# Kernel tuning notes

Measured on AMD Instinct MI355X. Metric: run time of the kernel, lower is better.

The kernel has to match this reference:

```python
import jax, jax.numpy as jnp
import numpy as np

N = 4096          # total atoms
N_METAL = 1024    # first N_METAL atoms are metal (Z=79) by construction
L = 24.0          # cubic cell edge (Angstrom)
DL = 2.4
NK = 10           # int(L / DL) -- static k-grid extent per axis
SIGMA = 1.0 / 1.805132
SCALING = 1.0
FOUR_PI = 4.0 * np.pi

# static integer reciprocal grid with k=0 removed: (K,3), K = (2*NK+1)^3 - 1
_g = np.arange(-NK, NK + 1)
_INTS = np.stack(np.meshgrid(_g, _g, _g, indexing="ij"), axis=-1).reshape(-1, 3)
_INTS = _INTS[np.any(_INTS != 0, axis=1)].astype(np.float32)


def _ewald_potential(r, q, cell):
    """Reciprocal-space Ewald potential at each atom position.
    r: (n,3) positions, q: (n,m) charges (m charge columns), cell: (3,3)
    rows = lattice vectors. Returns (n,m) potential ('field' f in cace).
    pot_i = (4*pi/V) * sum_k exp(-sigma^2 k^2/2)/k^2 * Re[S(k) e^{-ik.r_i}]."""
    recip = (2.0 * np.pi) * jnp.linalg.inv(cell).T      # rows b1,b2,b3
    k = jnp.asarray(_INTS, dtype=r.dtype) @ recip       # (K,3)
    k2 = jnp.sum(k * k, axis=1)                         # (K,)
    kfac = jnp.exp((-0.5 * SIGMA * SIGMA) * k2) / k2    # (K,)
    vol = jnp.abs(jnp.linalg.det(cell))
    kr = r @ k.T                                        # (n,K)  dominant alloc
    c, s = jnp.cos(kr), jnp.sin(kr)
    sf_c = c.T @ q                                      # (K,m) structure factors
    sf_s = s.T @ q
    pot = c @ (kfac[:, None] * sf_c) + s @ (kfac[:, None] * sf_s)
    return (FOUR_PI / vol) * pot


def setup_inputs() -> dict:
    key = jax.random.key(0)
    k1, k2 = jax.random.split(key)
    positions = jax.random.uniform(k1, (N, 3), dtype=jnp.float32) * L
    q = jax.random.normal(k2, (N, 1), dtype=jnp.float32) * 0.1
    cell = (L * jnp.eye(3, dtype=jnp.float32)).reshape(1, 3, 3)
    atomic_numbers = jnp.concatenate([
        jnp.full((N_METAL,), 79, dtype=jnp.int32),   # metal block first
        jnp.full((N - N_METAL,), 8, dtype=jnp.int32),
    ])
    batch = jnp.zeros((N,), dtype=jnp.int32)         # single system
    return {"positions": positions, "q": q, "cell": cell,
            "atomic_numbers": atomic_numbers, "batch": batch}


def reference(positions, q, cell, atomic_numbers, batch):
    # single batch (batch all zeros); metal atoms are the first N_METAL
    # (atomic_numbers == 79 by construction, so the boolean mask is static)
    cell0 = cell.reshape(3, 3)
    q = q.at[:N_METAL].set(0.0)                      # q_all[metal] = 0
    r_m = positions[:N_METAL]

    # _compute_S_matrix: pairwise Ewald kernel among metal atoms via q=eye
    A = _ewald_potential(r_m, jnp.eye(N_METAL, dtype=positions.dtype), cell0)
    coeffs = jnp.ones((N_METAL + 1, N_METAL + 1), dtype=positions.dtype)
    coeffs = coeffs.at[:N_METAL, :N_METAL].set(A)
    coeffs = coeffs.at[N_METAL, N_METAL].set(0.0)
    S = jnp.linalg.inv(coeffs)                       # cached AJl in torch code

    # field at every atom from all (electrolyte) charges
    f = _ewald_potential(positions, q, cell0)        # (N,1)

    # external_field is None -> B_ext = 0, no external energy
    B = -f[:N_METAL] * SCALING                       # (N_METAL,1)
    chi = jnp.concatenate([B, jnp.zeros((1, 1), dtype=B.dtype)], axis=0)
    sol = S @ chi                                    # (N_METAL+1,1)
    q_mw = q.at[:N_METAL].set(sol[:-1] / SCALING)
    return q_mw
```

## Files before the change

### kernel.cpp

```cpp
#include <hip/hip_runtime.h>
#include <math.h>

#define NATOM 4096
#define NM    1024
#define NKR   9260
#define KSPLIT 14
#define CHPS  22
#define NCH   308
#define KC    32
#define KPAD2 9856
#define PI_F  3.14159265358979f

typedef short v8s __attribute__((ext_vector_type(8)));
typedef float v4f __attribute__((ext_vector_type(4)));

static __device__ __forceinline__ void kdata(int t, const float* __restrict__ cell,
                                             float& kxx, float& kyy, float& kzz, float& w) {
  if (t >= NKR) { kxx = 0.f; kyy = 0.f; kzz = 0.f; w = 0.f; return; }
  int u = (t < 4630) ? t : t + 1;
  int a = u / 441;
  int rem = u - a * 441;
  int b = rem / 21;
  int c = rem - b * 21;
  float na = (float)(a - 10), nb = (float)(b - 10), nc = (float)(c - 10);
  float m00=cell[0], m01=cell[1], m02=cell[2];
  float m10=cell[3], m11=cell[4], m12=cell[5];
  float m20=cell[6], m21=cell[7], m22=cell[8];
  float det = m00*(m11*m22 - m12*m21) - m01*(m10*m22 - m12*m20) + m02*(m10*m21 - m11*m20);
  float inv00 =  (m11*m22 - m12*m21) / det;
  float inv01 = -(m01*m22 - m02*m21) / det;
  float inv02 =  (m01*m12 - m02*m11) / det;
  float inv10 = -(m10*m22 - m12*m20) / det;
  float inv11 =  (m00*m22 - m02*m20) / det;
  float inv12 = -(m00*m12 - m02*m10) / det;
  float inv20 =  (m10*m21 - m11*m20) / det;
  float inv21 = -(m00*m21 - m01*m20) / det;
  float inv22 =  (m00*m11 - m01*m10) / det;
  const float twopi = 2.f * PI_F;
  kxx = twopi * (na*inv00 + nb*inv01 + nc*inv02);
  kyy = twopi * (na*inv10 + nb*inv11 + nc*inv12);
  kzz = twopi * (na*inv20 + nb*inv21 + nc*inv22);
  float k2 = kxx*kxx + kyy*kyy + kzz*kzz;
  const float sigma = 1.0f / 1.805132f;
  w = (4.f * PI_F / fabsf(det)) * __expf(-0.5f * sigma * sigma * k2) / k2;
}

__global__ __launch_bounds__(256)
void sfk(const float* __restrict__ pos, const float* __restrict__ q,
         const float* __restrict__ cell,
         float* __restrict__ kx, float* __restrict__ ky,
         float* __restrict__ kz, float* __restrict__ ksw,
         float* __restrict__ gc, float* __restrict__ gs) {
  __shared__ float red1[8][32], red2[8][32];
  const int kloc = threadIdx.x & 31;
  const int part = threadIdx.x >> 5;
  const int k = blockIdx.x * 32 + kloc;
  float kxx, kyy, kzz, w;
  kdata(k, cell, kxx, kyy, kzz, w);
  if (part == 0) { kx[k]=kxx; ky[k]=kyy; kz[k]=kzz; ksw[k]=sqrtf(w); }
  float sc = 0.f, ss = 0.f;
  const int j0 = NM + part * 384, j1 = j0 + 384;
  for (int j = j0; j < j1; ++j) {
    float kr = kxx*pos[3*j] + kyy*pos[3*j+1] + kzz*pos[3*j+2];
    float s, c;
    __sincosf(kr, &s, &c);
    float qj = q[j];
    sc += qj * c;
    ss += qj * s;
  }
  red1[part][kloc] = sc;
  red2[part][kloc] = ss;
  __syncthreads();
  if (part == 0) {
    float tc = 0.f, ts = 0.f;
    #pragma unroll
    for (int pp = 0; pp < 8; ++pp) { tc += red1[pp][kloc]; ts += red2[pp][kloc]; }
    gc[k] = w * tc;
    gs[k] = w * ts;
  }
}

__global__ __launch_bounds__(256)
void fB(const float* __restrict__ pos,
        const float* __restrict__ kx, const float* __restrict__ ky,
        const float* __restrict__ kz,
        const float* __restrict__ gc, const float* __restrict__ gs,
        float* __restrict__ r1, float* __restrict__ r2) {
  int i = blockIdx.x;
  float px = pos[3*i], py = pos[3*i+1], pz = pos[3*i+2];
  float p = 0.f;
  for (int k = threadIdx.x; k < KPAD2; k += 256) {
    float kr = kx[k]*px + ky[k]*py + kz[k]*pz;
    float s, c;
    __sincosf(kr, &s, &c);
    p += gc[k]*c + gs[k]*s;
  }
  for (int o = 32; o > 0; o >>= 1) p += __shfl_down(p, o, 64);
  __shared__ float red[4];
  if ((threadIdx.x & 63) == 0) red[threadIdx.x >> 6] = p;
  __syncthreads();
  if (threadIdx.x == 0) {
    r1[i] = -(red[0] + red[1] + red[2] + red[3]);
    r2[i] = 1.f;
  }
}

#define PSTR 40
__global__ __launch_bounds__(256, 2)
void gemmA(const float* __restrict__ pos,
           const float* __restrict__ kx, const float* __restrict__ ky,
           const float* __restrict__ kz, const float* __restrict__ ksw,
           float* __restrict__ A) {
  __shared__ short Pl[8][128 * PSTR];
  const int blk = blockIdx.x;
  const int split = blk / 36;
  const int tt = blk - split * 36;
  int bi = 0, rem = tt;
  while (rem >= 8 - bi) { rem -= 8 - bi; ++bi; }
  const int bj = bi + rem;
  const int t = threadIdx.x;
  const int side = t >> 7;
  const int a = t & 127;
  const int atom = (side ? bj : bi) * 128 + a;
  const float px = pos[3*atom], py = pos[3*atom+1], pz = pos[3*atom+2];
  const int axor = (a >> 3) & 3;
  short* PC_hi = &Pl[side*4+0][a*PSTR];
  short* PC_mi = &Pl[side*4+1][a*PSTR];
  short* PS_hi = &Pl[side*4+2][a*PSTR];
  short* PS_mi = &Pl[side*4+3][a*PSTR];

  const int w = t >> 6;
  const int lane = t & 63;
  const int ln15 = lane & 15;
  const int quad = lane >> 4;

  v4f acc[2][8];
  #pragma unroll
  for (int mt = 0; mt < 2; ++mt)
    #pragma unroll
    for (int nt = 0; nt < 8; ++nt) {
      v4f z = {0.f, 0.f, 0.f, 0.f};
      acc[mt][nt] = z;
    }

  for (int ch = split * CHPS; ch < split * CHPS + CHPS; ++ch) {
    const int kb = ch * KC;
    #pragma unroll
    for (int g = 0; g < 4; ++g) {
      v8s vch, vcm, vsh, vsm;
      #pragma unroll
      for (int j = 0; j < 8; ++j) {
        const int gk = kb + g*8 + j;
        float kr = kx[gk]*px + ky[gk]*py + kz[gk]*pz;
        float s, c;
        __sincosf(kr, &s, &c);
        float sw = ksw[gk];
        float cv = c * sw, sv = s * sw;
        unsigned cu = __float_as_uint(cv);
        float chf = __uint_as_float(cu & 0xffff0000u);
        unsigned cmu = __float_as_uint(cv - chf);
        unsigned su = __float_as_uint(sv);
        float shf = __uint_as_float(su & 0xffff0000u);
        unsigned smu = __float_as_uint(sv - shf);
        vch[j] = (short)(cu >> 16);
        vcm[j] = (short)(cmu >> 16);
        vsh[j] = (short)(su >> 16);
        vsm[j] = (short)(smu >> 16);
      }
      const int slot = (g ^ axor) * 8;
      *(v8s*)&PC_hi[slot] = vch;
      *(v8s*)&PC_mi[slot] = vcm;
      *(v8s*)&PS_hi[slot] = vsh;
      *(v8s*)&PS_mi[slot] = vsm;
    }
    __syncthreads();
    v8s aCh[2], aCm[2], aSh[2], aSm[2];
    #pragma unroll
    for (int mt = 0; mt < 2; ++mt) {
      const int row = w*32 + mt*16 + ln15;
      const int off = row * PSTR + (quad ^ ((row >> 3) & 3)) * 8;
      aCh[mt] = *(const v8s*)&Pl[0][off];
      aCm[mt] = *(const v8s*)&Pl[1][off];
      aSh[mt] = *(const v8s*)&Pl[2][off];
      aSm[mt] = *(const v8s*)&Pl[3][off];
    }
    #pragma unroll
    for (int nt = 0; nt < 8; ++nt) {
      const int row = nt*16 + ln15;
      const int off = row * PSTR + (quad ^ ((row >> 3) & 3)) * 8;
      v8s bCh = *(const v8s*)&Pl[4][off];
      v8s bCm = *(const v8s*)&Pl[5][off];
      v8s bSh = *(const v8s*)&Pl[6][off];
      v8s bSm = *(const v8s*)&Pl[7][off];
      #pragma unroll
      for (int mt = 0; mt < 2; ++mt) {
        v4f d = acc[mt][nt];
        d = __builtin_amdgcn_mfma_f32_16x16x32_bf16(aCh[mt], bCh, d, 0, 0, 0);
        d = __builtin_amdgcn_mfma_f32_16x16x32_bf16(aCh[mt], bCm, d, 0, 0, 0);
        d = __builtin_amdgcn_mfma_f32_16x16x32_bf16(aCm[mt], bCh, d, 0, 0, 0);
        d = __builtin_amdgcn_mfma_f32_16x16x32_bf16(aSh[mt], bSh, d, 0, 0, 0);
        d = __builtin_amdgcn_mfma_f32_16x16x32_bf16(aSh[mt], bSm, d, 0, 0, 0);
        d = __builtin_amdgcn_mfma_f32_16x16x32_bf16(aSm[mt], bSh, d, 0, 0, 0);
        acc[mt][nt] = d;
      }
    }
    __syncthreads();
  }
  #pragma unroll
  for (int mt = 0; mt < 2; ++mt)
    #pragma unroll
    for (int nt = 0; nt < 8; ++nt)
      #pragma unroll
      for (int r = 0; r < 4; ++r) {
        const int row = bi*128 + w*32 + mt*16 + quad*4 + r;
        const int col = bj*128 + nt*16 + ln15;
        atomicAdd(&A[row*1024 + col], acc[mt][nt][r]);
      }
}

__global__ __launch_bounds__(256)
void step(float* __restrict__ A, const float* __restrict__ r1, const float* __restrict__ r2,
          float* __restrict__ ru1, float* __restrict__ ru2,
          float* __restrict__ y1g, float* __restrict__ y2g, int p) {
  __shared__ __align__(16) float D[32][36];
  __shared__ __align__(16) float T[32][36];
  __shared__ float yp1[32], yp2[32];
  const int t = threadIdx.x;
  const int nb = 32 - p;
  const int i0 = (t >> 4) * 2, j0 = (t & 15) * 2;
  const int lr = t >> 3, lc = (t & 7) * 4;

  if ((int)blockIdx.x >= nb) {
    int rem = blockIdx.x - nb, a = 0;
    while (rem >= a + 1) { rem -= (a + 1); ++a; }
    const int qi = p + 1 + a, qj = p + 1 + rem;
    *(v4f*)&D[lr][lc] = *(const v4f*)&A[(qi*32+lr)*1024 + (p-1)*32 + lc];
    *(v4f*)&T[lr][lc] = *(const v4f*)&A[(qj*32+lr)*1024 + (p-1)*32 + lc];
    float o[2][2];
    if (p == 1 && (qi >> 2) != (qj >> 2)) {
      #pragma unroll
      for (int ii = 0; ii < 2; ++ii)
        #pragma unroll
        for (int jj = 0; jj < 2; ++jj)
          o[ii][jj] = A[(qj*32 + j0+jj)*1024 + qi*32 + i0+ii];
    } else {
      #pragma unroll
      for (int ii = 0; ii < 2; ++ii)
        #pragma unroll
        for (int jj = 0; jj < 2; ++jj)
          o[ii][jj] = A[(qi*32+i0+ii)*1024 + qj*32 + j0+jj];
    }
    __syncthreads();
    for (int m = 0; m < 32; ++m) {
      float a0 = D[i0][m], a1 = D[i0+1][m];
      float b0 = T[j0][m], b1 = T[j0+1][m];
      o[0][0]-=a0*b0; o[0][1]-=a0*b1;
      o[1][0]-=a1*b0; o[1][1]-=a1*b1;
    }
    #pragma unroll
    for (int ii = 0; ii < 2; ++ii)
      #pragma unroll
      for (int jj = 0; jj < 2; ++jj)
        A[(qi*32+i0+ii)*1024 + qj*32 + j0+jj] = o[ii][jj];
    return;
  }

  const int b = blockIdx.x;
  const int q = p + b;
  float rv1 = 0.f, rv2 = 0.f;
  if (p >= 1 && t < 32) { yp1[t] = y1g[(p-1)*32 + t]; yp2[t] = y2g[(p-1)*32 + t]; }
  if (p == 0) {
    *(v4f*)&D[lr][lc] = *(const v4f*)&A[lr*1024 + lc];
    if (b > 0) {
      if (q < 4) {
        *(v4f*)&T[lr][lc] = *(const v4f*)&A[(q*32+lr)*1024 + lc];
      } else {
        for (int e = t; e < 1024; e += 256)
          T[e&31][e>>5] = A[(e>>5)*1024 + q*32 + (e&31)];
      }
    }
    __syncthreads();
    if (b == 0 && t < 32) { rv1 = r1[t]; rv2 = r2[t]; }
  } else {
    *(v4f*)&D[lr][lc] = *(const v4f*)&A[(p*32+lr)*1024 + (p-1)*32 + lc];
    if (b > 0)
      *(v4f*)&T[lr][lc] = *(const v4f*)&A[(q*32+lr)*1024 + (p-1)*32 + lc];
    __syncthreads();
    if (t < 32) {
      if (b == 0) {
        float a1 = 0.f, a2 = 0.f;
        for (int j = 0; j < 32; ++j) {
          float lv = D[t][j];
          a1 += lv * yp1[j];
          a2 += lv * yp2[j];
        }
        rv1 = r1[p*32 + t] - a1;
        rv2 = r2[p*32 + t] - a2;
      } else {
        float a1 = 0.f, a2 = 0.f;
        for (int j = 0; j < 32; ++j) {
          float lv = T[t][j];
          a1 += lv * yp1[j];
          a2 += lv * yp2[j];
        }
        ru1[q*32 + t] -= a1;
        ru2[q*32 + t] -= a2;
      }
    }
    float o1[2][2];
    #pragma unroll
    for (int ii = 0; ii < 2; ++ii)
      #pragma unroll
      for (int jj = 0; jj < 2; ++jj)
        o1[ii][jj] = A[(p*32+i0+ii)*1024 + p*32 + j0+jj];
    for (int m = 0; m < 32; ++m) {
      float a0 = D[i0][m], a1 = D[i0+1][m];
      float b0 = D[j0][m], b1 = D[j0+1][m];
      o1[0][0]-=a0*b0; o1[0][1]-=a0*b1;
      o1[1][0]-=a1*b0; o1[1][1]-=a1*b1;
    }
    float o2[2][2];
    if (b > 0) {
      if (p == 1 && (q >> 2) != 0) {
        #pragma unroll
        for (int ii = 0; ii < 2; ++ii)
          #pragma unroll
          for (int jj = 0; jj < 2; ++jj)
            o2[ii][jj] = A[(1*32 + j0+jj)*1024 + q*32 + i0+ii];
      } else {
        #pragma unroll
        for (int ii = 0; ii < 2; ++ii)
          #pragma unroll
          for (int jj = 0; jj < 2; ++jj)
            o2[ii][jj] = A[(q*32+i0+ii)*1024 + p*32 + j0+jj];
      }
      for (int m = 0; m < 32; ++m) {
        float a0 = T[i0][m], a1 = T[i0+1][m];
        float b0 = D[j0][m], b1 = D[j0+1][m];
        o2[0][0]-=a0*b0; o2[0][1]-=a0*b1;
        o2[1][0]-=a1*b0; o2[1][1]-=a1*b1;
      }
    }
    __syncthreads();
    #pragma unroll
    for (int ii = 0; ii < 2; ++ii)
      #pragma unroll
      for (int jj = 0; jj < 2; ++jj)
        D[i0+ii][j0+jj] = o1[ii][jj];
    if (b > 0) {
      #pragma unroll
      for (int ii = 0; ii < 2; ++ii)
        #pragma unroll
        for (int jj = 0; jj < 2; ++jj)
          T[i0+ii][j0+jj] = o2[ii][jj];
    }
    __syncthreads();
  }

  if (t < 32) {
    float a[32];
    #pragma unroll
    for (int m = 0; m < 32; ++m) a[m] = D[t][m];
    #pragma unroll
    for (int j = 0; j < 32; ++j) {
      float dj = __shfl(a[j], j);
      float rinv = rsqrtf(dj);
      float lj = (t == j) ? dj * rinv : a[j] * rinv;
      a[j] = lj;
      #pragma unroll
      for (int m = j + 1; m < 32; ++m)
        a[m] -= lj * __shfl(lj, m);
    }
    #pragma unroll
    for (int m = 0; m < 32; ++m) D[t][m] = a[m];
  }
  __syncthreads();
  if (b == 0) {
    for (int e = t; e < 1024; e += 256) {
      int i = e >> 5, j = e & 31;
      if (i >= j) A[(p*32+i)*1024 + p*32 + j] = D[i][j];
    }
    if (t < 32) {
      float v1 = rv1, v2 = rv2;
      for (int j = 0; j < 32; ++j) {
        float invd = 1.f / D[j][j];
        float Lij = D[t][j];
        float x1 = __shfl(v1, j) * invd;
        float x2 = __shfl(v2, j) * invd;
        if (t == j)      { v1 = x1; v2 = x2; }
        else if (t > j)  { v1 -= Lij * x1; v2 -= Lij * x2; }
      }
      y1g[p*32 + t] = v1; y2g[p*32 + t] = v2;
    }
  } else {
    if (t < 32) {
      #pragma unroll
      for (int cb = 0; cb < 2; ++cb) {
        const int cbase = cb * 16;
        float x[16];
        #pragma unroll
        for (int k = 0; k < 16; ++k) x[k] = T[t][cbase + k];
        for (int m = 0; m < cbase; ++m) {
          float tm = T[t][m];
          #pragma unroll
          for (int k = 0; k < 16; ++k)
            x[k] -= tm * D[cbase + k][m];
        }
        #pragma unroll
        for (int k = 0; k < 16; ++k) {
          float xv = x[k] * (1.0f / D[cbase + k][cbase + k]);
          x[k] = xv;
          #pragma unroll
          for (int m2 = k + 1; m2 < 16; ++m2)
            x[m2] -= xv * D[cbase + m2][cbase + k];
        }
        #pragma unroll
        for (int k = 0; k < 16; ++k) T[t][cbase + k] = x[k];
      }
    }
    __syncthreads();
    *(v4f*)&A[(q*32+lr)*1024 + p*32 + lc] = *(const v4f*)&T[lr][lc];
  }
}

__global__ __launch_bounds__(64)
void invd(const float* __restrict__ A, float* __restrict__ iD) {
  __shared__ float Lb[64][65];
  __shared__ float Xs[64][65];
  const int k = blockIdx.x;
  const int j = threadIdx.x;
  const int base = k * 64;
  for (int e = j; e < 4096; e += 64) {
    int r = e >> 6, c = e & 63;
    Lb[r][c] = (r >= c) ? A[(base + r)*1024 + base + c] : 0.f;
  }
  __syncthreads();
  for (int r = 0; r < j; ++r) Xs[r][j] = 0.f;
  Xs[j][j] = 1.f / Lb[j][j];
  for (int r = j + 1; r < 64; ++r) {
    float s = 0.f;
    for (int m = j; m < r; ++m) s += Lb[r][m] * Xs[m][j];
    Xs[r][j] = -s / Lb[r][r];
  }
  __syncthreads();
  for (int e = j; e < 4096; e += 64)
    iD[k*4096 + e] = Xs[e>>6][e&63];
}

__global__ __launch_bounds__(1024)
void bwd_out(const float* __restrict__ A, const float* __restrict__ iD,
             float* __restrict__ y1g, float* __restrict__ y2g,
             const float* __restrict__ qin, float* __restrict__ out) {
  __shared__ float D[64][65];
  __shared__ float yin1[64], yin2[64];
  __shared__ float x1s[64], x2s[64];
  __shared__ float rs1[16], rs2[16];
  const int t = threadIdx.x;
  for (int p = 15; p >= 0; --p) {
    const int base = p * 64;
    for (int e = t; e < 4096; e += 1024)
      D[e>>6][e&63] = iD[p*4096 + e];
    if (t < 64) { yin1[t] = y1g[base + t]; yin2[t] = y2g[base + t]; }
    __syncthreads();
    if (t < 64) {
      float v1 = 0.f, v2 = 0.f;
      #pragma unroll 8
      for (int m = 0; m < 64; ++m) {
        float w = D[m][t];
        v1 += w * yin1[m];
        v2 += w * yin2[m];
      }
      y1g[base + t] = v1; y2g[base + t] = v2;
      x1s[t] = v1; x2s[t] = v2;
    }
    __syncthreads();
    for (int rr = t; rr < base; rr += 1024) {
      float a1 = 0.f, a2 = 0.f;
      #pragma unroll 8
      for (int jj = 0; jj < 64; ++jj) {
        float lv = A[(base+jj)*1024 + rr];
        a1 += lv * x1s[jj];
        a2 += lv * x2s[jj];
      }
      y1g[rr] -= a1; y2g[rr] -= a2;
    }
    __syncthreads();
  }
  float s1 = y1g[t], s2 = y2g[t];
  for (int o = 32; o > 0; o >>= 1) { s1 += __shfl_down(s1, o, 64); s2 += __shfl_down(s2, o, 64); }
  if ((t & 63) == 0) { rs1[t >> 6] = s1; rs2[t >> 6] = s2; }
  __syncthreads();
  if (t == 0) {
    float a = 0.f, bb = 0.f;
    #pragma unroll
    for (int w = 0; w < 16; ++w) { a += rs1[w]; bb += rs2[w]; }
    rs1[0] = a / bb;
  }
  __syncthreads();
  const float lam = rs1[0];
  out[t] = y1g[t] - lam * y2g[t];
  for (int e = NM + t; e < NATOM; e += 1024) out[e] = qin[e];
}

extern "C" void kernel_launch(void* const* d_in, const int* in_sizes, int n_in,
                              void* d_out, int out_size, void* d_ws, size_t ws_size,
                              hipStream_t stream) {
  const float* pos  = (const float*)d_in[0];
  const float* q    = (const float*)d_in[1];
  const float* cell = (const float*)d_in[2];
  float* out = (float*)d_out;

  float* ws  = (float*)d_ws;
  float* A   = ws;
  float* kx  = ws + 1048576;
  float* ky  = kx + KPAD2;
  float* kz  = ky + KPAD2;
  float* ksw = kz + KPAD2;
  float* gc  = ksw + KPAD2;
  float* gs  = gc + KPAD2;
  float* r1  = gs + KPAD2;
  float* r2  = r1 + 1024;
  float* y1g = r2 + 1024;
  float* y2g = y1g + 1024;
  float* iD  = y2g + 1024;

  sfk<<<NCH, 256, 0, stream>>>(pos, q, cell, kx, ky, kz, ksw, gc, gs);
  fB<<<NM, 256, 0, stream>>>(pos, kx, ky, kz, gc, gs, r1, r2);
  hipMemsetAsync(A, 0, 1024 * 1024 * sizeof(float), stream);
  gemmA<<<36 * KSPLIT, 256, 0, stream>>>(pos, kx, ky, kz, ksw, A);
  for (int p = 0; p < 32; ++p) {
    const int s = 31 - p;
    const int grid = (32 - p) + ((p >= 1) ? s * (s + 1) / 2 : 0);
    step<<<grid, 256, 0, stream>>>(A, r1, r2, r1, r2, y1g, y2g, p);
  }
  invd<<<16, 64, 0, stream>>>(A, iD);
  bwd_out<<<1, 1024, 0, stream>>>(A, iD, y1g, y2g, q, out);
}
```

Before: 787.9 us.

## Fuse Cholesky panel steps into one persistent kernel with grid barriers

Replaces the 32 per-panel step launches of the blocked Cholesky factorization with a single persistent kernel of 256 blocks. Panels are separated by a software grid barrier built on device-scope atomics, and the trailing-update tiles are distributed round-robin across the blocks left idle by the panel work. This removes per-launch overhead and launch gaps. In exchange it needs all 256 blocks resident at once, adds spin-wait barrier latency, and reuses the iD buffer as barrier storage; the barrier loop has a spin cap that could break correctness if it is hit.

```diff
diff --git a/kernel.cpp b/kernel.cpp
--- a/kernel.cpp
+++ b/kernel.cpp
@@ -10,6 +10,7 @@
 #define KC    32
 #define KPAD2 9856
 #define PI_F  3.14159265358979f
+#define FGRID 256
 
 typedef short v8s __attribute__((ext_vector_type(8)));
 typedef float v4f __attribute__((ext_vector_type(4)));
@@ -218,208 +219,240 @@
       }
 }
 
-__global__ __launch_bounds__(256)
-void step(float* __restrict__ A, const float* __restrict__ r1, const float* __restrict__ r2,
-          float* __restrict__ ru1, float* __restrict__ ru2,
-          float* __restrict__ y1g, float* __restrict__ y2g, int p) {
+static __device__ __forceinline__ void gridbar(unsigned* bar) {
+  __syncthreads();
+  if (threadIdx.x == 0) {
+    __threadfence();
+    unsigned g = __hip_atomic_load(&bar[1], __ATOMIC_RELAXED, __HIP_MEMORY_SCOPE_AGENT);
+    unsigned a = __hip_atomic_fetch_add(&bar[0], 1u, __ATOMIC_ACQ_REL, __HIP_MEMORY_SCOPE_AGENT);
+    if (a == (unsigned)(FGRID - 1)) {
+      __hip_atomic_store(&bar[0], 0u, __ATOMIC_RELAXED, __HIP_MEMORY_SCOPE_AGENT);
+      __hip_atomic_store(&bar[1], g + 1u, __ATOMIC_RELEASE, __HIP_MEMORY_SCOPE_AGENT);
+    } else {
+      int spins = 0;
+      while (__hip_atomic_load(&bar[1], __ATOMIC_ACQUIRE, __HIP_MEMORY_SCOPE_AGENT) == g) {
+        __builtin_amdgcn_s_sleep(32);
+        if (++spins > 100000) break;
+      }
+    }
+    __threadfence();
+  }
+  __syncthreads();
+}
+
+__global__ __launch_bounds__(256, 2)
+void factor(float* __restrict__ A, float* __restrict__ r1, float* __restrict__ r2,
+            float* __restrict__ y1g, float* __restrict__ y2g, unsigned* bar) {
   __shared__ __align__(16) float D[32][36];
   __shared__ __align__(16) float T[32][36];
   __shared__ float yp1[32], yp2[32];
   const int t = threadIdx.x;
-  const int nb = 32 - p;
   const int i0 = (t >> 4) * 2, j0 = (t & 15) * 2;
   const int lr = t >> 3, lc = (t & 7) * 4;
 
-  if ((int)blockIdx.x >= nb) {
-    int rem = blockIdx.x - nb, a = 0;
-    while (rem >= a + 1) { rem -= (a + 1); ++a; }
-    const int qi = p + 1 + a, qj = p + 1 + rem;
-    *(v4f*)&D[lr][lc] = *(const v4f*)&A[(qi*32+lr)*1024 + (p-1)*32 + lc];
-    *(v4f*)&T[lr][lc] = *(const v4f*)&A[(qj*32+lr)*1024 + (p-1)*32 + lc];
-    float o[2][2];
-    if (p == 1 && (qi >> 2) != (qj >> 2)) {
+  for (int p = 0; p < 32; ++p) {
+    if (p) gridbar(bar);
+    const int nb = 32 - p;
+
+    if ((int)blockIdx.x >= nb) {
+      if (p >= 1) {
+        const int s = 31 - p;
+        const int ntile = s * (s + 1) / 2;
+        const int nsy = FGRID - nb;
+        for (int tile = (int)blockIdx.x - nb; tile < ntile; tile += nsy) {
+          int rem = tile, a = 0;
+          while (rem >= a + 1) { rem -= (a + 1); ++a; }
+          const int qi = p + 1 + a, qj = p + 1 + rem;
+          *(v4f*)&D[lr][lc] = *(const v4f*)&A[(qi*32+lr)*1024 + (p-1)*32 + lc];
+          *(v4f*)&T[lr][lc] = *(const v4f*)&A[(qj*32+lr)*1024 + (p-1)*32 + lc];
+          float o[2][2];
+          if (p == 1 && (qi >> 2) != (qj >> 2)) {
+            #pragma unroll
+            for (int ii = 0; ii < 2; ++ii)
+              #pragma unroll
+              for (int jj = 0; jj < 2; ++jj)
+                o[ii][jj] = A[(qj*32 + j0+jj)*1024 + qi*32 + i0+ii];
+          } else {
+            #pragma unroll
+            for (int ii = 0; ii < 2; ++ii)
+              #pragma unroll
+              for (int jj = 0; jj < 2; ++jj)
+                o[ii][jj] = A[(qi*32+i0+ii)*1024 + qj*32 + j0+jj];
+          }
+          __syncthreads();
+          for (int m = 0; m < 32; ++m) {
+            float a0 = D[i0][m], a1 = D[i0+1][m];
+            float b0 = T[j0][m], b1 = T[j0+1][m];
+            o[0][0]-=a0*b0; o[0][1]-=a0*b1;
+            o[1][0]-=a1*b0; o[1][1]-=a1*b1;
+          }
+          #pragma unroll
+          for (int ii = 0; ii < 2; ++ii)
+            #pragma unroll
+            for (int jj = 0; jj < 2; ++jj)
+              A[(qi*32+i0+ii)*1024 + qj*32 + j0+jj] = o[ii][jj];
+          __syncthreads();
+        }
+      }
+      continue;
+    }
+
+    const int b = blockIdx.x;
+    const int q = p + b;
+    float rv1 = 0.f, rv2 = 0.f;
+    if (p >= 1 && t < 32) { yp1[t] = y1g[(p-1)*32 + t]; yp2[t] = y2g[(p-1)*32 + t]; }
+    if (p == 0) {
+      *(v4f*)&D[lr][lc] = *(const v4f*)&A[lr*1024 + lc];
+      if (b > 0) {
+        if (q < 4) {
+          *(v4f*)&T[lr][lc] = *(const v4f*)&A[(q*32+lr)*1024 + lc];
+        } else {
+          for (int e = t; e < 1024; e += 256)
+            T[e&31][e>>5] = A[(e>>5)*1024 + q*32 + (e&31)];
+        }
+      }
+      __syncthreads();
+      if (b == 0 && t < 32) { rv1 = r1[t]; rv2 = r2[t]; }
+    } else {
+      *(v4f*)&D[lr][lc] = *(const v4f*)&A[(p*32+lr)*1024 + (p-1)*32 + lc];
+      if (b > 0)
+        *(v4f*)&T[lr][lc] = *(const v4f*)&A[(q*32+lr)*1024 + (p-1)*32 + lc];
+      __syncthreads();
+      if (t < 32) {
+        if (b == 0) {
+          float a1 = 0.f, a2 = 0.f;
+          for (int j = 0; j < 32; ++j) {
+            float lv = D[t][j];
+            a1 += lv * yp1[j];
+            a2 += lv * yp2[j];
+          }
+          rv1 = r1[p*32 + t] - a1;
+          rv2 = r2[p*32 + t] - a2;
+        } else {
+          float a1 = 0.f, a2 = 0.f;
+          for (int j = 0; j < 32; ++j) {
+            float lv = T[t][j];
+            a1 += lv * yp1[j];
+            a2 += lv * yp2[j];
+          }
+          r1[q*32 + t] -= a1;
+          r2[q*32 + t] -= a2;
+        }
+      }
+      float o1[2][2];
       #pragma unroll
       for (int ii = 0; ii < 2; ++ii)
         #pragma unroll
         for (int jj = 0; jj < 2; ++jj)
-          o[ii][jj] = A[(qj*32 + j0+jj)*1024 + qi*32 + i0+ii];
-    } else {
+          o1[ii][jj] = A[(p*32+i0+ii)*1024 + p*32 + j0+jj];
+      for (int m = 0; m < 32; ++m) {
+        float a0 = D[i0][m], a1 = D[i0+1][m];
+        float b0 = D[j0][m], b1 = D[j0+1][m];
+        o1[0][0]-=a0*b0; o1[0][1]-=a0*b1;
+        o1[1][0]-=a1*b0; o1[1][1]-=a1*b1;
+      }
+      float o2[2][2];
+      if (b > 0) {
+        if (p == 1 && (q >> 2) != 0) {
+          #pragma unroll
+          for (int ii = 0; ii < 2; ++ii)
+            #pragma unroll
+            for (int jj = 0; jj < 2; ++jj)
+              o2[ii][jj] = A[(1*32 + j0+jj)*1024 + q*32 + i0+ii];
+        } else {
+          #pragma unroll
+          for (int ii = 0; ii < 2; ++ii)
+            #pragma unroll
+            for (int jj = 0; jj < 2; ++jj)
+              o2[ii][jj] = A[(q*32+i0+ii)*1024 + p*32 + j0+jj];
+        }
+        for (int m = 0; m < 32; ++m) {
+          float a0 = T[i0][m], a1 = T[i0+1][m];
+          float b0 = D[j0][m], b1 = D[j0+1][m];
+          o2[0][0]-=a0*b0; o2[0][1]-=a0*b1;
+          o2[1][0]-=a1*b0; o2[1][1]-=a1*b1;
+        }
+      }
+      __syncthreads();
       #pragma unroll
       for (int ii = 0; ii < 2; ++ii)
         #pragma unroll
         for (int jj = 0; jj < 2; ++jj)
-          o[ii][jj] = A[(qi*32+i0+ii)*1024 + qj*32 + j0+jj];
-    }
-    __syncthreads();
-    for (int m = 0; m < 32; ++m) {
-      float a0 = D[i0][m], a1 = D[i0+1][m];
-      float b0 = T[j0][m], b1 = T[j0+1][m];
-      o[0][0]-=a0*b0; o[0][1]-=a0*b1;
-      o[1][0]-=a1*b0; o[1][1]-=a1*b1;
-    }
-    #pragma unroll
-    for (int ii = 0; ii < 2; ++ii)
-      #pragma unroll
-      for (int jj = 0; jj < 2; ++jj)
-        A[(qi*32+i0+ii)*1024 + qj*32 + j0+jj] = o[ii][jj];
-    return;
-  }
-
-  const int b = blockIdx.x;
-  const int q = p + b;
-  float rv1 = 0.f, rv2 = 0.f;
-  if (p >= 1 && t < 32) { yp1[t] = y1g[(p-1)*32 + t]; yp2[t] = y2g[(p-1)*32 + t]; }
-  if (p == 0) {
-    *(v4f*)&D[lr][lc] = *(const v4f*)&A[lr*1024 + lc];
-    if (b > 0) {
-      if (q < 4) {
-        *(v4f*)&T[lr][lc] = *(const v4f*)&A[(q*32+lr)*1024 + lc];
-      } else {
-        for (int e = t; e < 1024; e += 256)
-          T[e&31][e>>5] = A[(e>>5)*1024 + q*32 + (e&31)];
-      }
-    }
-    __syncthreads();
-    if (b == 0 && t < 32) { rv1 = r1[t]; rv2 = r2[t]; }
-  } else {
-    *(v4f*)&D[lr][lc] = *(const v4f*)&A[(p*32+lr)*1024 + (p-1)*32 + lc];
-    if (b > 0)
-      *(v4f*)&T[lr][lc] = *(const v4f*)&A[(q*32+lr)*1024 + (p-1)*32 + lc];
-    __syncthreads();
-    if (t < 32) {
-      if (b == 0) {
-        float a1 = 0.f, a2 = 0.f;
-        for (int j = 0; j < 32; ++j) {
-          float lv = D[t][j];
-          a1 += lv * yp1[j];
-          a2 += lv * yp2[j];
-        }
-        rv1 = r1[p*32 + t] - a1;
-        rv2 = r2[p*32 + t] - a2;
-      } else {
-        float a1 = 0.f, a2 = 0.f;
-        for (int j = 0; j < 32; ++j) {
-          float lv = T[t][j];
-          a1 += lv * yp1[j];
-          a2 += lv * yp2[j];
-        }
-        ru1[q*32 + t] -= a1;
-        ru2[q*32 + t] -= a2;
-      }
-    }
-    float o1[2][2];
-    #pragma unroll
-    for (int ii = 0; ii < 2; ++ii)
-      #pragma unroll
-      for (int jj = 0; jj < 2; ++jj)
-        o1[ii][jj] = A[(p*32+i0+ii)*1024 + p*32 + j0+jj];
-    for (int m = 0; m < 32; ++m) {
-      float a0 = D[i0][m], a1 = D[i0+1][m];
-      float b0 = D[j0][m], b1 = D[j0+1][m];
-      o1[0][0]-=a0*b0; o1[0][1]-=a0*b1;
-      o1[1][0]-=a1*b0; o1[1][1]-=a1*b1;
-    }
-    float o2[2][2];
-    if (b > 0) {
-      if (p == 1 && (q >> 2) != 0) {
+          D[i0+ii][j0+jj] = o1[ii][jj];
+      if (b > 0) {
         #pragma unroll
         for (int ii = 0; ii < 2; ++ii)
           #pragma unroll
           for (int jj = 0; jj < 2; ++jj)
-            o2[ii][jj] = A[(1*32 + j0+jj)*1024 + q*32 + i0+ii];
-      } else {
+            T[i0+ii][j0+jj] = o2[ii][jj];
+      }
+      __syncthreads();
+    }
+
+    if (t < 32) {
+      float a[32];
+      #pragma unroll
+      for (int m = 0; m < 32; ++m) a[m] = D[t][m];
+      #pragma unroll
+      for (int j = 0; j < 32; ++j) {
+        float dj = __shfl(a[j], j);
+        float rinv = rsqrtf(dj);
+        float lj = (t == j) ? dj * rinv : a[j] * rinv;
+        a[j] = lj;
         #pragma unroll
-        for (int ii = 0; ii < 2; ++ii)
-          #pragma unroll
-          for (int jj = 0; jj < 2; ++jj)
-            o2[ii][jj] = A[(q*32+i0+ii)*1024 + p*32 + j0+jj];
-      }
-      for (int m = 0; m < 32; ++m) {
-        float a0 = T[i0][m], a1 = T[i0+1][m];
-        float b0 = D[j0][m], b1 = D[j0+1][m];
-        o2[0][0]-=a0*b0; o2[0][1]-=a0*b1;
-        o2[1][0]-=a1*b0; o2[1][1]-=a1*b1;
-      }
+        for (int m = j + 1; m < 32; ++m)
+          a[m] -= lj * __shfl(lj, m);
+      }
+      #pragma unroll
+      for (int m = 0; m < 32; ++m) D[t][m] = a[m];
     }
     __syncthreads();
-    #pragma unroll
-    for (int ii = 0; ii < 2; ++ii)
-      #pragma unroll
-      for (int jj = 0; jj < 2; ++jj)
-        D[i0+ii][j0+jj] = o1[ii][jj];
-    if (b > 0) {
-      #pragma unroll
-      for (int ii = 0; ii < 2; ++ii)
+    if (b == 0) {
+      for (int e = t; e < 1024; e += 256) {
+        int i = e >> 5, j = e & 31;
+        if (i >= j) A[(p*32+i)*1024 + p*32 + j] = D[i][j];
+      }
+      if (t < 32) {
+        float v1 = rv1, v2 = rv2;
+        for (int j = 0; j < 32; ++j) {
+          float invd = 1.f / D[j][j];
+          float Lij = D[t][j];
+          float x1 = __shfl(v1, j) * invd;
+          float x2 = __shfl(v2, j) * invd;
+          if (t == j)      { v1 = x1; v2 = x2; }
+          else if (t > j)  { v1 -= Lij * x1; v2 -= Lij * x2; }
+        }
+        y1g[p*32 + t] = v1; y2g[p*32 + t] = v2;
+      }
+    } else {
+      if (t < 32) {
         #pragma unroll
-        for (int jj = 0; jj < 2; ++jj)
-          T[i0+ii][j0+jj] = o2[ii][jj];
-    }
-    __syncthreads();
-  }
-
-  if (t < 32) {
-    float a[32];
-    #pragma unroll
-    for (int m = 0; m < 32; ++m) a[m] = D[t][m];
-    #pragma unroll
-    for (int j = 0; j < 32; ++j) {
-      float dj = __shfl(a[j], j);
-      float rinv = rsqrtf(dj);
-      float lj = (t == j) ? dj * rinv : a[j] * rinv;
-      a[j] = lj;
-      #pragma unroll
-      for (int m = j + 1; m < 32; ++m)
-        a[m] -= lj * __shfl(lj, m);
-    }
-    #pragma unroll
-    for (int m = 0; m < 32; ++m) D[t][m] = a[m];
-  }
-  __syncthreads();
-  if (b == 0) {
-    for (int e = t; e < 1024; e += 256) {
-      int i = e >> 5, j = e & 31;
-      if (i >= j) A[(p*32+i)*1024 + p*32 + j] = D[i][j];
-    }
-    if (t < 32) {
-      float v1 = rv1, v2 = rv2;
-      for (int j = 0; j < 32; ++j) {
-        float invd = 1.f / D[j][j];
-        float Lij = D[t][j];
-        float x1 = __shfl(v1, j) * invd;
-        float x2 = __shfl(v2, j) * invd;
-        if (t == j)      { v1 = x1; v2 = x2; }
-        else if (t > j)  { v1 -= Lij * x1; v2 -= Lij * x2; }
-      }
-      y1g[p*32 + t] = v1; y2g[p*32 + t] = v2;
-    }
-  } else {
-    if (t < 32) {
-      #pragma unroll
-      for (int cb = 0; cb < 2; ++cb) {
-        const int cbase = cb * 16;
-        float x[16];
-        #pragma unroll
-        for (int k = 0; k < 16; ++k) x[k] = T[t][cbase + k];
-        for (int m = 0; m < cbase; ++m) {
-          float tm = T[t][m];
-          #pragma unroll
-          for (int k = 0; k < 16; ++k)
-            x[k] -= tm * D[cbase + k][m];
-        }
-        #pragma unroll
-        for (int k = 0; k < 16; ++k) {
-          float xv = x[k] * (1.0f / D[cbase + k][cbase + k]);
-          x[k] = xv;
-          #pragma unroll
-          for (int m2 = k + 1; m2 < 16; ++m2)
-            x[m2] -= xv * D[cbase + m2][cbase + k];
-        }
-        #pragma unroll
-        for (int k = 0; k < 16; ++k) T[t][cbase + k] = x[k];
-      }
-    }
-    __syncthreads();
-    *(v4f*)&A[(q*32+lr)*1024 + p*32 + lc] = *(const v4f*)&T[lr][lc];
+        for (int cb = 0; cb < 2; ++cb) {
+          const int cbase = cb * 16;
+          float x[16];
+          #pragma unroll
+          for (int k = 0; k < 16; ++k) x[k] = T[t][cbase + k];
+          for (int m = 0; m < cbase; ++m) {
+            float tm = T[t][m];
+            #pragma unroll
+            for (int k = 0; k < 16; ++k)
+              x[k] -= tm * D[cbase + k][m];
+          }
+          #pragma unroll
+          for (int k = 0; k < 16; ++k) {
+            float xv = x[k] * (1.0f / D[cbase + k][cbase + k]);
+            x[k] = xv;
+            #pragma unroll
+            for (int m2 = k + 1; m2 < 16; ++m2)
+              x[m2] -= xv * D[cbase + m2][cbase + k];
+          }
+          #pragma unroll
+          for (int k = 0; k < 16; ++k) T[t][cbase + k] = x[k];
+        }
+      }
+      __syncthreads();
+      *(v4f*)&A[(q*32+lr)*1024 + p*32 + lc] = *(const v4f*)&T[lr][lc];
+    }
   }
 }
 
@@ -523,16 +556,16 @@
   float* y1g = r2 + 1024;
   float* y2g = y1g + 1024;
   float* iD  = y2g + 1024;
+  unsigned* bar = (unsigned*)iD;
 
   sfk<<<NCH, 256, 0, stream>>>(pos, q, cell, kx, ky, kz, ksw, gc, gs);
   fB<<<NM, 256, 0, stream>>>(pos, kx, ky, kz, gc, gs, r1, r2);
   hipMemsetAsync(A, 0, 1024 * 1024 * sizeof(float), stream);
+  hipMemsetAsync(bar, 0, 2 * sizeof(unsigned), stream);
   gemmA<<<36 * KSPLIT, 256, 0, stream>>>(pos, kx, ky, kz, ksw, A);
-  for (int p = 0; p < 32; ++p) {
-    const int s = 31 - p;
-    const int grid = (32 - p) + ((p >= 1) ? s * (s + 1) / 2 : 0);
-    step<<<grid, 256, 0, stream>>>(A, r1, r2, r1, r2, y1g, y2g, p);
-  }
+
+  factor<<<FGRID, 256, 0, stream>>>(A, r1, r2, y1g, y2g, bar);
+
   invd<<<16, 64, 0, stream>>>(A, iD);
   bwd_out<<<1, 1024, 0, stream>>>(A, iD, y1g, y2g, q, out);
 }
```

Measured after the change: 1.634 ms. +107.4%, slower.

## Fuse last twelve blocked Cholesky steps into one single-block tail kernel

Applied to the files above, without the earlier changes.

The last twelve panel steps of the blocked Cholesky factorization and forward solve, which were separate small kernel launches, now run inside one 1024-thread workgroup kernel. That kernel does the pending trailing update, then the diagonal factor, panel solve, RHS update and trailing update for each remaining block, with __syncthreads between phases. This removes per-launch overhead and underfilled grids on the small tail of the factorization. In exchange the whole tail runs on a single compute unit with serialized phases, and the workgroup carries register-heavy 8x8 tiles.

```diff
diff --git a/kernel.cpp b/kernel.cpp
--- a/kernel.cpp
+++ b/kernel.cpp
@@ -10,6 +10,7 @@
 #define KC    32
 #define KPAD2 9856
 #define PI_F  3.14159265358979f
+#define TAILP 20
 
 typedef short v8s __attribute__((ext_vector_type(8)));
 typedef float v4f __attribute__((ext_vector_type(4)));
@@ -423,6 +424,192 @@
   }
 }
 
+static __device__ __forceinline__ void chol32s(float (*Dl)[33], int t) {
+  float a[32];
+  #pragma unroll
+  for (int m = 0; m < 32; ++m) a[m] = Dl[t][m];
+  #pragma unroll
+  for (int j = 0; j < 32; ++j) {
+    float dj = __shfl(a[j], j);
+    float rinv = rsqrtf(dj);
+    float lj = (t == j) ? dj * rinv : a[j] * rinv;
+    a[j] = lj;
+    #pragma unroll
+    for (int m = j + 1; m < 32; ++m)
+      a[m] -= lj * __shfl(lj, m);
+  }
+  #pragma unroll
+  for (int m = 0; m < 32; ++m) Dl[t][m] = a[m];
+}
+
+__global__ __launch_bounds__(1024)
+void tailfactor(float* __restrict__ A, const float* __restrict__ r1, const float* __restrict__ r2,
+                float* __restrict__ y1g, float* __restrict__ y2g) {
+  __shared__ float Lc[12][32][33];
+  __shared__ float Dd[32][33];
+  __shared__ float rs1[384], rs2[384];
+  __shared__ float ys1[32], ys2[32];
+  const int t = threadIdx.x;
+  const int tg = t >> 4, tt = t & 15;
+  const int mi0 = (tt >> 2) * 8, mj0 = (tt & 3) * 8;
+
+  for (int e = t; e < 12 * 1024; e += 1024) {
+    int k = e >> 10, r = (e >> 5) & 31, c = e & 31;
+    Lc[k][r][c] = A[((TAILP + k) * 32 + r) * 1024 + (TAILP - 1) * 32 + c];
+  }
+  if (t < 32) { ys1[t] = y1g[(TAILP - 1) * 32 + t]; ys2[t] = y2g[(TAILP - 1) * 32 + t]; }
+  if (t >= 64 && t < 64 + 384) { rs1[t - 64] = r1[TAILP * 32 + t - 64]; rs2[t - 64] = r2[TAILP * 32 + t - 64]; }
+  __syncthreads();
+  if (t < 384) {
+    const int k = t >> 5, rr = t & 31;
+    float a1 = 0.f, a2 = 0.f;
+    #pragma unroll
+    for (int m = 0; m < 32; ++m) { float lv = Lc[k][rr][m]; a1 += lv * ys1[m]; a2 += lv * ys2[m]; }
+    rs1[t] -= a1; rs2[t] -= a2;
+  }
+  for (int tau = tg; tau < 78; tau += 64) {
+    int rem = tau, a = 0;
+    while (rem >= a + 1) { rem -= a + 1; ++a; }
+    const int bq = TAILP + a, bj = TAILP + rem;
+    float o[8][8];
+    #pragma unroll
+    for (int ii = 0; ii < 8; ++ii) {
+      v4f u0 = *(const v4f*)&A[(bq*32 + mi0+ii)*1024 + bj*32 + mj0];
+      v4f u1 = *(const v4f*)&A[(bq*32 + mi0+ii)*1024 + bj*32 + mj0 + 4];
+      o[ii][0]=u0[0]; o[ii][1]=u0[1]; o[ii][2]=u0[2]; o[ii][3]=u0[3];
+      o[ii][4]=u1[0]; o[ii][5]=u1[1]; o[ii][6]=u1[2]; o[ii][7]=u1[3];
+    }
+    for (int m = 0; m < 32; ++m) {
+      float av[8], bv[8];
+      #pragma unroll
+      for (int ii = 0; ii < 8; ++ii) av[ii] = Lc[a][mi0+ii][m];
+      #pragma unroll
+      for (int jj = 0; jj < 8; ++jj) bv[jj] = Lc[rem][mj0+jj][m];
+      #pragma unroll
+      for (int ii = 0; ii < 8; ++ii)
+        #pragma unroll
+        for (int jj = 0; jj < 8; ++jj)
+          o[ii][jj] -= av[ii] * bv[jj];
+    }
+    #pragma unroll
+    for (int ii = 0; ii < 8; ++ii) {
+      v4f u0 = {o[ii][0], o[ii][1], o[ii][2], o[ii][3]};
+      v4f u1 = {o[ii][4], o[ii][5], o[ii][6], o[ii][7]};
+      *(v4f*)&A[(bq*32 + mi0+ii)*1024 + bj*32 + mj0] = u0;
+      *(v4f*)&A[(bq*32 + mi0+ii)*1024 + bj*32 + mj0 + 4] = u1;
+    }
+  }
+  __syncthreads();
+
+  for (int i = TAILP; i < 32; ++i) {
+    const int m = 31 - i, nr = m * 32, ntile = m * (m + 1) / 2;
+    { int r = t >> 5, c = t & 31; if (t < 1024) Dd[r][c] = A[(i*32 + r)*1024 + i*32 + c]; }
+    __syncthreads();
+    if (t < 32) chol32s(Dd, t);
+    __syncthreads();
+    { int r = t >> 5, c = t & 31; if (t < 1024) A[(i*32 + r)*1024 + i*32 + c] = Dd[r][c]; }
+    if (t < 32) {
+      float v1 = rs1[(i - TAILP) * 32 + t], v2 = rs2[(i - TAILP) * 32 + t];
+      for (int j = 0; j < 32; ++j) {
+        float invd_ = 1.f / Dd[j][j];
+        float Lij = Dd[t][j];
+        float x1 = __shfl(v1, j) * invd_;
+        float x2 = __shfl(v2, j) * invd_;
+        if (t == j)      { v1 = x1; v2 = x2; }
+        else if (t > j)  { v1 -= Lij * x1; v2 -= Lij * x2; }
+      }
+      ys1[t] = v1; ys2[t] = v2;
+      y1g[i*32 + t] = v1; y2g[i*32 + t] = v2;
+    }
+    __syncthreads();
+    if (m == 0) break;
+    if (t < nr) {
+      const int kq = t >> 5, rr = t & 31;
+      float* gp = &A[((i + 1 + kq)*32 + rr)*1024 + i*32];
+      float x[32];
+      #pragma unroll
+      for (int c4 = 0; c4 < 8; ++c4) {
+        v4f u = *(const v4f*)&gp[c4*4];
+        x[c4*4+0]=u[0]; x[c4*4+1]=u[1]; x[c4*4+2]=u[2]; x[c4*4+3]=u[3];
+      }
+      #pragma unroll
+      for (int cb = 0; cb < 2; ++cb) {
+        const int cbase = cb * 16;
+        float xx[16];
+        #pragma unroll
+        for (int k = 0; k < 16; ++k) xx[k] = x[cbase + k];
+        if (cb == 1) {
+          #pragma unroll
+          for (int mm = 0; mm < 16; ++mm) {
+            float tm = x[mm];
+            #pragma unroll
+            for (int k = 0; k < 16; ++k) xx[k] -= tm * Dd[cbase + k][mm];
+          }
+        }
+        #pragma unroll
+        for (int k = 0; k < 16; ++k) {
+          float xv = xx[k] * (1.0f / Dd[cbase + k][cbase + k]);
+          xx[k] = xv;
+          #pragma unroll
+          for (int m2 = k + 1; m2 < 16; ++m2)
+            xx[m2] -= xv * Dd[cbase + m2][cbase + k];
+        }
+        #pragma unroll
+        for (int k = 0; k < 16; ++k) x[cbase + k] = xx[k];
+      }
+      #pragma unroll
+      for (int c4 = 0; c4 < 8; ++c4) {
+        v4f u = {x[c4*4+0], x[c4*4+1], x[c4*4+2], x[c4*4+3]};
+        *(v4f*)&gp[c4*4] = u;
+      }
+      #pragma unroll
+      for (int c = 0; c < 32; ++c) Lc[kq][rr][c] = x[c];
+    }
+    __syncthreads();
+    if (t < nr) {
+      const int kq = t >> 5, rr = t & 31;
+      float a1 = 0.f, a2 = 0.f;
+      #pragma unroll
+      for (int mm = 0; mm < 32; ++mm) { float lv = Lc[kq][rr][mm]; a1 += lv * ys1[mm]; a2 += lv * ys2[mm]; }
+      rs1[(i + 1 - TAILP) * 32 + t] -= a1;
+      rs2[(i + 1 - TAILP) * 32 + t] -= a2;
+    }
+    for (int tau = tg; tau < ntile; tau += 64) {
+      int rem = tau, a = 0;
+      while (rem >= a + 1) { rem -= a + 1; ++a; }
+      const int bq = i + 1 + a, bj = i + 1 + rem;
+      float o[8][8];
+      #pragma unroll
+      for (int ii = 0; ii < 8; ++ii) {
+        v4f u0 = *(const v4f*)&A[(bq*32 + mi0+ii)*1024 + bj*32 + mj0];
+        v4f u1 = *(const v4f*)&A[(bq*32 + mi0+ii)*1024 + bj*32 + mj0 + 4];
+        o[ii][0]=u0[0]; o[ii][1]=u0[1]; o[ii][2]=u0[2]; o[ii][3]=u0[3];
+        o[ii][4]=u1[0]; o[ii][5]=u1[1]; o[ii][6]=u1[2]; o[ii][7]=u1[3];
+      }
+      for (int mm = 0; mm < 32; ++mm) {
+        float av[8], bv[8];
+        #pragma unroll
+        for (int ii = 0; ii < 8; ++ii) av[ii] = Lc[a][mi0+ii][mm];
+        #pragma unroll
+        for (int jj = 0; jj < 8; ++jj) bv[jj] = Lc[rem][mj0+jj][mm];
+        #pragma unroll
+        for (int ii = 0; ii < 8; ++ii)
+          #pragma unroll
+          for (int jj = 0; jj < 8; ++jj)
+            o[ii][jj] -= av[ii] * bv[jj];
+      }
+      #pragma unroll
+      for (int ii = 0; ii < 8; ++ii) {
+        v4f u0 = {o[ii][0], o[ii][1], o[ii][2], o[ii][3]};
+        v4f u1 = {o[ii][4], o[ii][5], o[ii][6], o[ii][7]};
+        *(v4f*)&A[(bq*32 + mi0+ii)*1024 + bj*32 + mj0] = u0;
+        *(v4f*)&A[(bq*32 + mi0+ii)*1024 + bj*32 + mj0 + 4] = u1;
+      }
+    }
+    __syncthreads();
+  }
+}
+
 __global__ __launch_bounds__(64)
 void invd(const float* __restrict__ A, float* __restrict__ iD) {
   __shared__ float Lb[64][65];
@@ -528,11 +715,12 @@
   fB<<<NM, 256, 0, stream>>>(pos, kx, ky, kz, gc, gs, r1, r2);
   hipMemsetAsync(A, 0, 1024 * 1024 * sizeof(float), stream);
   gemmA<<<36 * KSPLIT, 256, 0, stream>>>(pos, kx, ky, kz, ksw, A);
-  for (int p = 0; p < 32; ++p) {
+  for (int p = 0; p < TAILP; ++p) {
     const int s = 31 - p;
     const int grid = (32 - p) + ((p >= 1) ? s * (s + 1) / 2 : 0);
     step<<<grid, 256, 0, stream>>>(A, r1, r2, r1, r2, y1g, y2g, p);
   }
+  tailfactor<<<1, 1024, 0, stream>>>(A, r1, r2, y1g, y2g);
   invd<<<16, 64, 0, stream>>>(A, iD);
   bwd_out<<<1, 1024, 0, stream>>>(A, iD, y1g, y2g, q, out);
 }
```

New measurement: 931.6 us. +18.2%, slower.

## Precompute split-bf16 trig panels once, stream them into the A-matrix GEMM

Applied to the files above, without the earlier changes.

Adds a kernel that evaluates sin/cos of k·r for every metal atom and k-chunk once and stores hi/lo bf16-split panels in workspace. A new GEMM variant then loads these panels instead of recomputing the transcendentals per tile pair, since the old kernel recomputed each atom's phases once for every tile pair it appeared in. The trade is roughly 80 MB of extra global memory traffic, and it falls back to the old path when the workspace is too small.

```diff
diff --git a/kernel.cpp b/kernel.cpp
--- a/kernel.cpp
+++ b/kernel.cpp
@@ -105,7 +105,138 @@
   }
 }
 
+__global__ __launch_bounds__(256)
+void sfP(const float* __restrict__ pos,
+         const float* __restrict__ kx, const float* __restrict__ ky,
+         const float* __restrict__ kz, const float* __restrict__ ksw,
+         short* __restrict__ P) {
+  const int ch = blockIdx.x >> 2;
+  const int atom = ((blockIdx.x & 3) << 8) + threadIdx.x;
+  const float px = pos[3*atom], py = pos[3*atom+1], pz = pos[3*atom+2];
+  const int kb = ch * KC;
+  const int base = ch * 4 * 32768 + atom * 32;
+  #pragma unroll
+  for (int g = 0; g < 4; ++g) {
+    v8s vch, vcm, vsh, vsm;
+    #pragma unroll
+    for (int j = 0; j < 8; ++j) {
+      const int gk = kb + g*8 + j;
+      float kr = kx[gk]*px + ky[gk]*py + kz[gk]*pz;
+      float s, c;
+      __sincosf(kr, &s, &c);
+      float sw = ksw[gk];
+      float cv = c * sw, sv = s * sw;
+      unsigned cu = __float_as_uint(cv);
+      float chf = __uint_as_float(cu & 0xffff0000u);
+      unsigned cmu = __float_as_uint(cv - chf);
+      unsigned su = __float_as_uint(sv);
+      float shf = __uint_as_float(su & 0xffff0000u);
+      unsigned smu = __float_as_uint(sv - shf);
+      vch[j] = (short)(cu >> 16);
+      vcm[j] = (short)(cmu >> 16);
+      vsh[j] = (short)(su >> 16);
+      vsm[j] = (short)(smu >> 16);
+    }
+    *(v8s*)&P[base + 0*32768 + g*8] = vch;
+    *(v8s*)&P[base + 1*32768 + g*8] = vcm;
+    *(v8s*)&P[base + 2*32768 + g*8] = vsh;
+    *(v8s*)&P[base + 3*32768 + g*8] = vsm;
+  }
+}
+
 #define PSTR 40
+__global__ __launch_bounds__(256, 2)
+void gemmAF(const short* __restrict__ P, float* __restrict__ A) {
+  __shared__ short Pl[8][128 * PSTR];
+  const int blk = blockIdx.x;
+  const int split = blk / 36;
+  const int tt = blk - split * 36;
+  int bi = 0, rem = tt;
+  while (rem >= 8 - bi) { rem -= 8 - bi; ++bi; }
+  const int bj = bi + rem;
+  const int t = threadIdx.x;
+  const int side = t >> 7;
+  const int a = t & 127;
+  const int atom = (side ? bj : bi) * 128 + a;
+  const int axor = (a >> 3) & 3;
+  short* PC_hi = &Pl[side*4+0][a*PSTR];
+  short* PC_mi = &Pl[side*4+1][a*PSTR];
+  short* PS_hi = &Pl[side*4+2][a*PSTR];
+  short* PS_mi = &Pl[side*4+3][a*PSTR];
+
+  const int w = t >> 6;
+  const int lane = t & 63;
+  const int ln15 = lane & 15;
+  const int quad = lane >> 4;
+
+  v4f acc[2][8];
+  #pragma unroll
+  for (int mt = 0; mt < 2; ++mt)
+    #pragma unroll
+    for (int nt = 0; nt < 8; ++nt) {
+      v4f z = {0.f, 0.f, 0.f, 0.f};
+      acc[mt][nt] = z;
+    }
+
+  for (int ch = split * CHPS; ch < split * CHPS + CHPS; ++ch) {
+    const int pb = ch * 4 * 32768 + atom * 32;
+    #pragma unroll
+    for (int g = 0; g < 4; ++g) {
+      v8s vch = *(const v8s*)&P[pb + 0*32768 + g*8];
+      v8s vcm = *(const v8s*)&P[pb + 1*32768 + g*8];
+      v8s vsh = *(const v8s*)&P[pb + 2*32768 + g*8];
+      v8s vsm = *(const v8s*)&P[pb + 3*32768 + g*8];
+      const int slot = (g ^ axor) * 8;
+      *(v8s*)&PC_hi[slot] = vch;
+      *(v8s*)&PC_mi[slot] = vcm;
+      *(v8s*)&PS_hi[slot] = vsh;
+      *(v8s*)&PS_mi[slot] = vsm;
+    }
+    __syncthreads();
+    v8s aCh[2], aCm[2], aSh[2], aSm[2];
+    #pragma unroll
+    for (int mt = 0; mt < 2; ++mt) {
+      const int row = w*32 + mt*16 + ln15;
+      const int off = row * PSTR + (quad ^ ((row >> 3) & 3)) * 8;
+      aCh[mt] = *(const v8s*)&Pl[0][off];
+      aCm[mt] = *(const v8s*)&Pl[1][off];
+      aSh[mt] = *(const v8s*)&Pl[2][off];
+      aSm[mt] = *(const v8s*)&Pl[3][off];
+    }
+    #pragma unroll
+    for (int nt = 0; nt < 8; ++nt) {
+      const int row = nt*16 + ln15;
+      const int off = row * PSTR + (quad ^ ((row >> 3) & 3)) * 8;
+      v8s bCh = *(const v8s*)&Pl[4][off];
+      v8s bCm = *(const v8s*)&Pl[5][off];
+      v8s bSh = *(const v8s*)&Pl[6][off];
+      v8s bSm = *(const v8s*)&Pl[7][off];
+      #pragma unroll
+      for (int mt = 0; mt < 2; ++mt) {
+        v4f d = acc[mt][nt];
+        d = __builtin_amdgcn_mfma_f32_16x16x32_bf16(aCh[mt], bCh, d, 0, 0, 0);
+        d = __builtin_amdgcn_mfma_f32_16x16x32_bf16(aCh[mt], bCm, d, 0, 0, 0);
+        d = __builtin_amdgcn_mfma_f32_16x16x32_bf16(aCm[mt], bCh, d, 0, 0, 0);
+        d = __builtin_amdgcn_mfma_f32_16x16x32_bf16(aSh[mt], bSh, d, 0, 0, 0);
+        d = __builtin_amdgcn_mfma_f32_16x16x32_bf16(aSh[mt], bSm, d, 0, 0, 0);
+        d = __builtin_amdgcn_mfma_f32_16x16x32_bf16(aSm[mt], bSh, d, 0, 0, 0);
+        acc[mt][nt] = d;
+      }
+    }
+    __syncthreads();
+  }
+  #pragma unroll
+  for (int mt = 0; mt < 2; ++mt)
+    #pragma unroll
+    for (int nt = 0; nt < 8; ++nt)
+      #pragma unroll
+      for (int r = 0; r < 4; ++r) {
+        const int row = bi*128 + w*32 + mt*16 + quad*4 + r;
+        const int col = bj*128 + nt*16 + ln15;
+        atomicAdd(&A[row*1024 + col], acc[mt][nt][r]);
+      }
+}
+
 __global__ __launch_bounds__(256, 2)
 void gemmA(const float* __restrict__ pos,
            const float* __restrict__ kx, const float* __restrict__ ky,
@@ -523,11 +654,21 @@
   float* y1g = r2 + 1024;
   float* y2g = y1g + 1024;
   float* iD  = y2g + 1024;
+  short* P   = (short*)(iD + 16 * 4096);
+
+  const size_t needBytes = (size_t)(1048576 + 6*KPAD2 + 4*1024 + 16*4096) * 4
+                         + (size_t)NCH * 4 * 32768 * 2;
+  const bool fast = (ws_size >= needBytes);
 
   sfk<<<NCH, 256, 0, stream>>>(pos, q, cell, kx, ky, kz, ksw, gc, gs);
   fB<<<NM, 256, 0, stream>>>(pos, kx, ky, kz, gc, gs, r1, r2);
   hipMemsetAsync(A, 0, 1024 * 1024 * sizeof(float), stream);
-  gemmA<<<36 * KSPLIT, 256, 0, stream>>>(pos, kx, ky, kz, ksw, A);
+  if (fast) {
+    sfP<<<NCH * 4, 256, 0, stream>>>(pos, kx, ky, kz, ksw, P);
+    gemmAF<<<36 * KSPLIT, 256, 0, stream>>>(P, A);
+  } else {
+    gemmA<<<36 * KSPLIT, 256, 0, stream>>>(pos, kx, ky, kz, ksw, A);
+  }
   for (int p = 0; p < 32; ++p) {
     const int s = 31 - p;
     const int grid = (32 - p) + ((p >= 1) ? s * (s + 1) / 2 : 0);
```

Result: slower. 826.8 us (+4.9%).
